# Optimization experiments

Hardware: AMD Instinct MI355X
Metric: run time of the kernel (lower is better)

The kernel has to match this reference:

```python
import jax, jax.numpy as jnp
import numpy as np

B, S, D, H = 8, 4096, 1024, 16
HD = D // H          # 64 head dim
NR = HD // 2         # 32 rotations
BASE = 10000.0


def setup_inputs() -> dict:
    key = jax.random.key(0)
    k0, k1, k2 = jax.random.split(key, 3)
    x = jax.random.normal(k0, (B, S, D), jnp.float32)
    thetas = jax.random.normal(k1, (NR,), jnp.float32) * 0.1
    r_pairs = jax.random.uniform(k2, (NR, 2), jnp.float32) * HD  # float indices in [0, HD)
    theta_scale = jnp.ones((1,), jnp.float32)
    n_rots_scale = jnp.ones((1,), jnp.float32)
    r_matrix = jnp.eye(HD, dtype=jnp.float32)
    inv_freq = 1.0 / (BASE ** (jnp.arange(0, HD, 2, dtype=jnp.float32) / HD))  # [HD/2]
    return {"x": x, "thetas": thetas, "r_pairs": r_pairs,
            "theta_scale": theta_scale, "n_rots_scale": n_rots_scale,
            "r_matrix": r_matrix, "inv_freq": inv_freq}


def reference(x, thetas, r_pairs, theta_scale, n_rots_scale, r_matrix, inv_freq):
    b, s, d = x.shape
    hd = r_matrix.shape[0]
    h = d // hd
    xf = x.reshape(-1, hd)  # [B*S*H, hd]

    # adjusted_n_rots = round(n_rots_scale * n_rots); n_rots_scale == 1 -> all rotations
    # (the int() in torch is non-differentiable/static anyway)
    idx = r_pairs.astype(jnp.int32)          # floor of non-negative floats, like .long()
    th = thetas * theta_scale[0]             # [NR]

    def step(xc, inp):
        i, j, t = inp
        c, sn = jnp.cos(t), jnp.sin(t)
        xi = xc[:, i]
        xj = xc[:, j]
        same = i == j
        # x @ G: col i -> xi*c + xj*s, col j -> -xi*s + xj*c; if i==j torch's
        # overwrite order leaves G[i,i] = cos -> col i = xi*c
        ni = jnp.where(same, xi * c, xi * c + xj * sn)
        nj = jnp.where(same, xi * c, -xi * sn + xj * c)
        xc = xc.at[:, i].set(ni)
        xc = xc.at[:, j].set(nj)
        return xc, None

    xf, _ = jax.lax.scan(step, xf, (idx[:, 0], idx[:, 1], th))
    xf = xf @ r_matrix                       # [B*S*H, hd]
    x4 = xf.reshape(b, s, h, hd)

    pos = jnp.arange(s, dtype=jnp.float32)
    sinusoid = pos[:, None] * inv_freq[None, :]        # [S, hd/2]
    sin = jnp.sin(sinusoid)[None, :, None, :]
    cos = jnp.cos(sinusoid)[None, :, None, :]
    x1 = x4[..., ::2]
    x2 = x4[..., 1::2]
    out = jnp.concatenate([x1 * cos - x2 * sin, x1 * sin + x2 * cos], axis=-1)
    return out.reshape(b, s, d)
```

## Files before the change

### kernel.cpp

```cpp
#include <hip/hip_runtime.h>
#include <hip/hip_bf16.h>

#define BB 8
#define SS 4096
#define DD 1024
#define HH 16
#define HD 64
#define NR 32
#define NROWS (BB * SS * HH)

__global__ __launch_bounds__(256) void build_C_kernel(
    const float* __restrict__ thetas,
    const float* __restrict__ r_pairs,
    const float* __restrict__ theta_scale,
    const float* __restrict__ r_matrix,
    float* __restrict__ C_out)
{
    __shared__ float W[64 * 68];
    __shared__ int   ii[NR], jj[NR];
    __shared__ float cc[NR], ss[NR];

    const int t = threadIdx.x;

#pragma unroll
    for (int it = 0; it < 16; ++it) {
        int idx = t + 256 * it;
        W[(idx >> 6) * 68 + (idx & 63)] = r_matrix[idx];
    }
    if (t < NR) {
        ii[t] = (int)r_pairs[2 * t];
        jj[t] = (int)r_pairs[2 * t + 1];
        float th = thetas[t] * theta_scale[0];
        cc[t] = cosf(th);
        ss[t] = sinf(th);
    }
    __syncthreads();

    if (t < 64) {
        for (int k = NR - 1; k >= 0; --k) {
            int i = ii[k], j = jj[k];
            float c = cc[k], s = ss[k];
            float xi = W[i * 68 + t];
            float xj = W[j * 68 + t];
            if (i == j) {
                W[i * 68 + t] = c * xi;
            } else {
                W[i * 68 + t] = c * xi - s * xj;
                W[j * 68 + t] = s * xi + c * xj;
            }
        }
    }
    __syncthreads();

#pragma unroll
    for (int it = 0; it < 16; ++it) {
        int idx = t + 256 * it;
        C_out[idx] = W[(idx >> 6) * 68 + (idx & 63)];
    }
}

#define RPB 128
#define XT_STRIDE 132

__global__ __launch_bounds__(256) void rope_main_kernel(
    const float* __restrict__ x,
    const float* __restrict__ C,
    const float* __restrict__ inv_freq,
    float* __restrict__ out)
{
    __shared__ float Cs[64 * 64];
    __shared__ float xT[64 * XT_STRIDE];

    const int t = threadIdx.x;
    const size_t tile = (size_t)blockIdx.x * (RPB * HD);

    {
        const float4* C4  = (const float4*)C;
        float4*       Cs4 = (float4*)Cs;
#pragma unroll
        for (int it = 0; it < 4; ++it)
            Cs4[t + 256 * it] = C4[t + 256 * it];
    }
    {
        const float4* x4 = (const float4*)(x + tile);
#pragma unroll
        for (int it = 0; it < 8; ++it) {
            int f = t + 256 * it;
            float4 v = x4[f];
            int row = f >> 4;
            int k4  = (f & 15) << 2;
            xT[(k4 + 0) * XT_STRIDE + row] = v.x;
            xT[(k4 + 1) * XT_STRIDE + row] = v.y;
            xT[(k4 + 2) * XT_STRIDE + row] = v.z;
            xT[(k4 + 3) * XT_STRIDE + row] = v.w;
        }
    }
    __syncthreads();

    const int jq = t & 7;
    const int rg = t >> 3;
    const int j0 = jq << 3;
    const int r0 = rg << 2;

    float acc[4][8];
#pragma unroll
    for (int u = 0; u < 4; ++u)
#pragma unroll
        for (int v = 0; v < 8; ++v) acc[u][v] = 0.0f;

#pragma unroll 4
    for (int k = 0; k < 64; ++k) {
        const float4 av  = *(const float4*)&xT[k * XT_STRIDE + r0];
        const float4 bv0 = *(const float4*)&Cs[(k << 6) + j0];
        const float4 bv1 = *(const float4*)&Cs[(k << 6) + j0 + 4];
        const float a[4] = {av.x, av.y, av.z, av.w};
        const float b[8] = {bv0.x, bv0.y, bv0.z, bv0.w, bv1.x, bv1.y, bv1.z, bv1.w};
#pragma unroll
        for (int u = 0; u < 4; ++u)
#pragma unroll
            for (int v = 0; v < 8; ++v)
                acc[u][v] = fmaf(a[u], b[v], acc[u][v]);
    }

    const size_t grow0 = (size_t)blockIdx.x * RPB + r0;
    const int   s_pos  = (int)((grow0 >> 4) & (SS - 1));
    const float pos    = (float)s_pos;

    const int rbase = j0 >> 1;
    const float4 invf = *(const float4*)&inv_freq[rbase];
    float cs[4], sn[4];
    __sincosf(pos * invf.x, &sn[0], &cs[0]);
    __sincosf(pos * invf.y, &sn[1], &cs[1]);
    __sincosf(pos * invf.z, &sn[2], &cs[2]);
    __sincosf(pos * invf.w, &sn[3], &cs[3]);

#pragma unroll
    for (int u = 0; u < 4; ++u) {
        float* orow = out + tile + (size_t)(r0 + u) * HD;
        float4 o1, o2;
        o1.x = acc[u][0] * cs[0] - acc[u][1] * sn[0];
        o1.y = acc[u][2] * cs[1] - acc[u][3] * sn[1];
        o1.z = acc[u][4] * cs[2] - acc[u][5] * sn[2];
        o1.w = acc[u][6] * cs[3] - acc[u][7] * sn[3];
        o2.x = acc[u][0] * sn[0] + acc[u][1] * cs[0];
        o2.y = acc[u][2] * sn[1] + acc[u][3] * cs[1];
        o2.z = acc[u][4] * sn[2] + acc[u][5] * cs[2];
        o2.w = acc[u][6] * sn[3] + acc[u][7] * cs[3];
        *(float4*)&orow[rbase]      = o1;
        *(float4*)&orow[32 + rbase] = o2;
    }
}

extern "C" void kernel_launch(void* const* d_in, const int* in_sizes, int n_in,
                              void* d_out, int out_size, void* d_ws, size_t ws_size,
                              hipStream_t stream)
{
    const float* x           = (const float*)d_in[0];
    const float* thetas      = (const float*)d_in[1];
    const float* r_pairs     = (const float*)d_in[2];
    const float* theta_scale = (const float*)d_in[3];
    const float* r_matrix    = (const float*)d_in[5];
    const float* inv_freq    = (const float*)d_in[6];
    float* out = (float*)d_out;
    float* Cws = (float*)d_ws;

    build_C_kernel<<<1, 256, 0, stream>>>(thetas, r_pairs, theta_scale, r_matrix, Cws);

    const int nblocks = NROWS / RPB;
    rope_main_kernel<<<nblocks, 256, 0, stream>>>(x, Cws, inv_freq, out);
}
```

Before: 250.1 us.

## Replace FP32 LDS GEMM with split-bf16 MFMA computed straight from registers

The 64x64 rotation-matrix multiply now runs on MFMA bf16 instructions instead of the scalar FMA loop. A three-term hi/lo bf16 split keeps accuracy close to fp32. The matrix is pre-packed into MFMA fragment layout by the setup kernel and held in registers, and x is loaded directly from global memory into fragments with a one-group register prefetch, so the LDS transpose and barriers go away. Output columns are permuted so the even/odd pairs for RoPE land in the same lane. The cost is extra split arithmetic and six MFMAs per tile, plus narrower float2 stores and a small accuracy risk from the bf16x3 approximation.

```diff
diff --git a/kernel.cpp b/kernel.cpp
--- a/kernel.cpp
+++ b/kernel.cpp
@@ -1,5 +1,4 @@
 #include <hip/hip_runtime.h>
-#include <hip/hip_bf16.h>
 
 #define BB 8
 #define SS 4096
@@ -8,17 +7,24 @@
 #define HD 64
 #define NR 32
 #define NROWS (BB * SS * HH)
+#define NGRP (NROWS / 16)
+#define GPW 4
+#define GPB (4 * GPW)
+#define NBLK (NGRP / GPB)
 
-__global__ __launch_bounds__(256) void build_C_kernel(
+typedef __attribute__((ext_vector_type(8))) short bf16x8;
+typedef __attribute__((ext_vector_type(4))) float f32x4;
+
+__global__ __launch_bounds__(256) void build_pack_kernel(
     const float* __restrict__ thetas,
     const float* __restrict__ r_pairs,
     const float* __restrict__ theta_scale,
     const float* __restrict__ r_matrix,
-    float* __restrict__ C_out)
+    unsigned short* __restrict__ Apack)
 {
     __shared__ float W[64 * 68];
     __shared__ int   ii[NR], jj[NR];
-    __shared__ float cc[NR], ss[NR];
+    __shared__ float cc[NR], ssn[NR];
 
     const int t = threadIdx.x;
 
@@ -31,15 +37,15 @@
         ii[t] = (int)r_pairs[2 * t];
         jj[t] = (int)r_pairs[2 * t + 1];
         float th = thetas[t] * theta_scale[0];
-        cc[t] = cosf(th);
-        ss[t] = sinf(th);
+        cc[t]  = cosf(th);
+        ssn[t] = sinf(th);
     }
     __syncthreads();
 
     if (t < 64) {
         for (int k = NR - 1; k >= 0; --k) {
             int i = ii[k], j = jj[k];
-            float c = cc[k], s = ss[k];
+            float c = cc[k], s = ssn[k];
             float xi = W[i * 68 + t];
             float xj = W[j * 68 + t];
             if (i == j) {
@@ -54,100 +60,116 @@
 
 #pragma unroll
     for (int it = 0; it < 16; ++it) {
-        int idx = t + 256 * it;
-        C_out[idx] = W[(idx >> 6) * 68 + (idx & 63)];
+        int flat = t + 256 * it;
+        int j    = flat & 7;
+        int lane = (flat >> 3) & 63;
+        int ks   = (flat >> 9) & 1;
+        int tt   = flat >> 10;
+        int i    = tt * 16 + (lane & 15);
+        int k    = ks * 32 + ((lane >> 4) << 3) + j;
+        float v  = W[k * 68 + i];
+        unsigned u  = __float_as_uint(v);
+        unsigned uh = u & 0xFFFF0000u;
+        float fl    = v - __uint_as_float(uh);
+        Apack[flat]        = (unsigned short)(uh >> 16);
+        Apack[4096 + flat] = (unsigned short)(__float_as_uint(fl) >> 16);
     }
 }
 
-#define RPB 128
-#define XT_STRIDE 132
+__device__ __forceinline__ void split8(const float4 a, const float4 b,
+                                       bf16x8& hi, bf16x8& lo)
+{
+    const float f[8] = {a.x, a.y, a.z, a.w, b.x, b.y, b.z, b.w};
+#pragma unroll
+    for (int j = 0; j < 8; ++j) {
+        unsigned u  = __float_as_uint(f[j]);
+        unsigned uh = u & 0xFFFF0000u;
+        hi[j] = (short)(uh >> 16);
+        float fl = f[j] - __uint_as_float(uh);
+        lo[j] = (short)(__float_as_uint(fl) >> 16);
+    }
+}
 
-__global__ __launch_bounds__(256) void rope_main_kernel(
+__global__ __launch_bounds__(256, 3) void rope_mfma_kernel(
     const float* __restrict__ x,
-    const float* __restrict__ C,
+    const unsigned short* __restrict__ Apack,
     const float* __restrict__ inv_freq,
     float* __restrict__ out)
 {
-    __shared__ float Cs[64 * 64];
-    __shared__ float xT[64 * XT_STRIDE];
+    const int lane = threadIdx.x & 63;
+    const int wv   = threadIdx.x >> 6;
+    const int q    = lane >> 4;
+    const int rr   = lane & 15;
 
-    const int t = threadIdx.x;
-    const size_t tile = (size_t)blockIdx.x * (RPB * HD);
+    bf16x8 Ah[4][2], Al[4][2];
+    {
+        const bf16x8* Ap = (const bf16x8*)Apack;
+#pragma unroll
+        for (int tt = 0; tt < 4; ++tt)
+#pragma unroll
+            for (int ks = 0; ks < 2; ++ks) {
+                Ah[tt][ks] = Ap[(tt * 2 + ks) * 64 + lane];
+                Al[tt][ks] = Ap[512 + (tt * 2 + ks) * 64 + lane];
+            }
+    }
+    float2 invf[4];
+#pragma unroll
+    for (int tt = 0; tt < 4; ++tt)
+        invf[tt] = *(const float2*)&inv_freq[tt * 8 + q * 2];
 
-    {
-        const float4* C4  = (const float4*)C;
-        float4*       Cs4 = (float4*)Cs;
+    int g = blockIdx.x * GPB + wv * GPW;
+
+    const float* xr = x + ((size_t)g * 16 + rr) * 64 + q * 8;
+    float4 fa0 = *(const float4*)(xr);
+    float4 fa1 = *(const float4*)(xr + 4);
+    float4 fa2 = *(const float4*)(xr + 32);
+    float4 fa3 = *(const float4*)(xr + 36);
+
+#pragma unroll 1
+    for (int gi = 0; gi < GPW; ++gi, ++g) {
+        float4 fb0 = fa0, fb1 = fa1, fb2 = fa2, fb3 = fa3;
+        if (gi + 1 < GPW) {
+            const float* xn = x + ((size_t)(g + 1) * 16 + rr) * 64 + q * 8;
+            fb0 = *(const float4*)(xn);
+            fb1 = *(const float4*)(xn + 4);
+            fb2 = *(const float4*)(xn + 32);
+            fb3 = *(const float4*)(xn + 36);
+        }
+
+        bf16x8 Bh0, Bl0, Bh1, Bl1;
+        split8(fa0, fa1, Bh0, Bl0);
+        split8(fa2, fa3, Bh1, Bl1);
+
+        f32x4 acc[4];
 #pragma unroll
-        for (int it = 0; it < 4; ++it)
-            Cs4[t + 256 * it] = C4[t + 256 * it];
-    }
-    {
-        const float4* x4 = (const float4*)(x + tile);
+        for (int tt = 0; tt < 4; ++tt) {
+            f32x4 a = {0.f, 0.f, 0.f, 0.f};
+            a = __builtin_amdgcn_mfma_f32_16x16x32_bf16(Ah[tt][0], Bh0, a, 0, 0, 0);
+            a = __builtin_amdgcn_mfma_f32_16x16x32_bf16(Ah[tt][1], Bh1, a, 0, 0, 0);
+            a = __builtin_amdgcn_mfma_f32_16x16x32_bf16(Al[tt][0], Bh0, a, 0, 0, 0);
+            a = __builtin_amdgcn_mfma_f32_16x16x32_bf16(Al[tt][1], Bh1, a, 0, 0, 0);
+            a = __builtin_amdgcn_mfma_f32_16x16x32_bf16(Ah[tt][0], Bl0, a, 0, 0, 0);
+            a = __builtin_amdgcn_mfma_f32_16x16x32_bf16(Ah[tt][1], Bl1, a, 0, 0, 0);
+            acc[tt] = a;
+        }
+
+        const float pos = (float)(g & (SS - 1));
+        float* orow = out + ((size_t)g * 16 + rr) * 64;
 #pragma unroll
-        for (int it = 0; it < 8; ++it) {
-            int f = t + 256 * it;
-            float4 v = x4[f];
-            int row = f >> 4;
-            int k4  = (f & 15) << 2;
-            xT[(k4 + 0) * XT_STRIDE + row] = v.x;
-            xT[(k4 + 1) * XT_STRIDE + row] = v.y;
-            xT[(k4 + 2) * XT_STRIDE + row] = v.z;
-            xT[(k4 + 3) * XT_STRIDE + row] = v.w;
+        for (int tt = 0; tt < 4; ++tt) {
+            float sn0, cs0, sn1, cs1;
+            __sincosf(pos * invf[tt].x, &sn0, &cs0);
+            __sincosf(pos * invf[tt].y, &sn1, &cs1);
+            const float y0 = acc[tt][0], y1 = acc[tt][1];
+            const float y2 = acc[tt][2], y3 = acc[tt][3];
+            const int m0 = tt * 8 + q * 2;
+            float2 o1 = { y0 * cs0 - y1 * sn0, y2 * cs1 - y3 * sn1 };
+            float2 o2 = { y0 * sn0 + y1 * cs0, y2 * sn1 + y3 * cs1 };
+            *(float2*)&orow[m0]      = o1;
+            *(float2*)&orow[32 + m0] = o2;
         }
-    }
-    __syncthreads();
 
-    const int jq = t & 7;
-    const int rg = t >> 3;
-    const int j0 = jq << 3;
-    const int r0 = rg << 2;
-
-    float acc[4][8];
-#pragma unroll
-    for (int u = 0; u < 4; ++u)
-#pragma unroll
-        for (int v = 0; v < 8; ++v) acc[u][v] = 0.0f;
-
-#pragma unroll 4
-    for (int k = 0; k < 64; ++k) {
-        const float4 av  = *(const float4*)&xT[k * XT_STRIDE + r0];
-        const float4 bv0 = *(const float4*)&Cs[(k << 6) + j0];
-        const float4 bv1 = *(const float4*)&Cs[(k << 6) + j0 + 4];
-        const float a[4] = {av.x, av.y, av.z, av.w};
-        const float b[8] = {bv0.x, bv0.y, bv0.z, bv0.w, bv1.x, bv1.y, bv1.z, bv1.w};
-#pragma unroll
-        for (int u = 0; u < 4; ++u)
-#pragma unroll
-            for (int v = 0; v < 8; ++v)
-                acc[u][v] = fmaf(a[u], b[v], acc[u][v]);
-    }
-
-    const size_t grow0 = (size_t)blockIdx.x * RPB + r0;
-    const int   s_pos  = (int)((grow0 >> 4) & (SS - 1));
-    const float pos    = (float)s_pos;
-
-    const int rbase = j0 >> 1;
-    const float4 invf = *(const float4*)&inv_freq[rbase];
-    float cs[4], sn[4];
-    __sincosf(pos * invf.x, &sn[0], &cs[0]);
-    __sincosf(pos * invf.y, &sn[1], &cs[1]);
-    __sincosf(pos * invf.z, &sn[2], &cs[2]);
-    __sincosf(pos * invf.w, &sn[3], &cs[3]);
-
-#pragma unroll
-    for (int u = 0; u < 4; ++u) {
-        float* orow = out + tile + (size_t)(r0 + u) * HD;
-        float4 o1, o2;
-        o1.x = acc[u][0] * cs[0] - acc[u][1] * sn[0];
-        o1.y = acc[u][2] * cs[1] - acc[u][3] * sn[1];
-        o1.z = acc[u][4] * cs[2] - acc[u][5] * sn[2];
-        o1.w = acc[u][6] * cs[3] - acc[u][7] * sn[3];
-        o2.x = acc[u][0] * sn[0] + acc[u][1] * cs[0];
-        o2.y = acc[u][2] * sn[1] + acc[u][3] * cs[1];
-        o2.z = acc[u][4] * sn[2] + acc[u][5] * cs[2];
-        o2.w = acc[u][6] * sn[3] + acc[u][7] * cs[3];
-        *(float4*)&orow[rbase]      = o1;
-        *(float4*)&orow[32 + rbase] = o2;
+        fa0 = fb0; fa1 = fb1; fa2 = fb2; fa3 = fb3;
     }
 }
 
@@ -162,10 +184,9 @@
     const float* r_matrix    = (const float*)d_in[5];
     const float* inv_freq    = (const float*)d_in[6];
     float* out = (float*)d_out;
-    float* Cws = (float*)d_ws;
+    unsigned short* Apack = (unsigned short*)d_ws;
 
-    build_C_kernel<<<1, 256, 0, stream>>>(thetas, r_pairs, theta_scale, r_matrix, Cws);
-
-    const int nblocks = NROWS / RPB;
-    rope_main_kernel<<<nblocks, 256, 0, stream>>>(x, Cws, inv_freq, out);
+    build_pack_kernel<<<1, 256, 0, stream>>>(thetas, r_pairs, theta_scale,
+                                             r_matrix, Apack);
+    rope_mfma_kernel<<<NBLK, 256, 0, stream>>>(x, Apack, inv_freq, out);
 }
```

New measurement: 259.4 us. 1.04x slower.
